# Kernel optimization log

Hardware: AMD Instinct MI355X
Metric: run time of the kernel (lower is better)

Reference implementation:

```python
import jax, jax.numpy as jnp
import numpy as np
from jax import lax

K = 100  # self.k in the module


def setup_inputs() -> dict:
    key = jax.random.key(0)
    k1, k2 = jax.random.split(key)
    query_batch = jax.random.normal(k1, (4, 64, 128), dtype=jnp.float32)  # [B,T,Z]
    targets = jax.random.normal(k2, (100000, 128), dtype=jnp.float32)     # [M,Z]
    return {"query_batch": query_batch, "targets": targets}


def _knn_emissions(query_batch, targets):
    # Brute-force L2 kNN (faiss.IndexFlatL2.search equivalent).
    # sqdist[b,t,m] = ||q_bt - target_m||^2
    qn = jnp.sum(query_batch * query_batch, -1)          # [B,T]
    tn = jnp.sum(targets * targets, -1)                  # [M]
    dots = jnp.einsum('btz,mz->btm', query_batch, targets)
    sqdist = qn[..., None] + tn[None, None, :] - 2.0 * dots  # [B,T,M]
    neg_d, idx = lax.top_k(-sqdist, K)                   # k smallest distances
    distances = -neg_d                                   # [B,T,K]
    # probabilities = exp(-d) / sum exp(-d)  == softmax(-d)
    emit_p = jax.nn.softmax(-distances, axis=-1)         # [B,T,K]
    states = targets[idx]                                # [B,T,K,Z]
    return emit_p, states


def _transition_probs(states):
    # Banded transitions: only between the K states of step t and step t+1.
    # transition_probability(a, b) = exp(-||a-b||^2)  (Gaussian L2 kernel)
    a = states[:, :-1]                                   # [B,T-1,K,Z]
    b = states[:, 1:]                                    # [B,T-1,K,Z]
    d = jnp.sum(a * a, -1)[..., :, None] + jnp.sum(b * b, -1)[..., None, :] \
        - 2.0 * jnp.einsum('btiz,btjz->btij', a, b)      # [B,T-1,K,K]
    return jnp.exp(-d)


def _viterbi_single(emit_p, trans_p):
    # emit_p [T,K], trans_p [T-1,K,K] -> best path indices [T] (int32)
    v0 = emit_p[0]

    def step(v, inp):
        tr, em = inp                                     # [K,K], [K]
        scores = v[:, None] * tr                         # [K,K]
        best = scores.max(axis=0)
        back = jnp.argmax(scores, axis=0)                # [K]
        v_new = best * em
        # rescale to avoid underflow over long T; argmax path unchanged
        v_new = v_new / jnp.maximum(v_new.max(), jnp.float32(1e-30))
        return v_new, back

    v_last, backptrs = lax.scan(step, v0, (trans_p, emit_p[1:]))
    last = jnp.argmax(v_last).astype(jnp.int32)

    def back_step(idx, bp):
        prev = bp[idx].astype(jnp.int32)
        return prev, prev

    _, path_head = lax.scan(back_step, last, backptrs, reverse=True)  # [T-1]
    return jnp.concatenate([path_head, last[None]])      # [T]


def reference(query_batch, targets):
    emit_p, states = _knn_emissions(query_batch, targets)
    trans_p = _transition_probs(states)
    paths = jax.vmap(_viterbi_single)(emit_p, trans_p)   # [B,T]
    # gather selected reference states: [B,T,Z]
    out = jnp.take_along_axis(states, paths[..., None, None], axis=2)[:, :, 0, :]
    return out
```

## Files before the change

kernel.cpp:

```cpp
#include <hip/hip_runtime.h>
#include <cfloat>
#include <climits>
#include <cstdint>
#include <cstddef>

#define ZD    128
#define NQ    256
#define NB    4
#define NT    64
#define KK    100
#define CAP   2048
#define NSAMP 4096
#define RANK  24
#define EPS   3.0f
#define SLABS 256
#define BKT   24
#define TROWS 64
#define QROWS 128
#define LPAD  136

typedef __attribute__((ext_vector_type(8))) short  short8;
typedef __attribute__((ext_vector_type(4))) float  floatx4;
typedef unsigned long long u64;

__device__ inline unsigned short f2bf(float f) {
  unsigned u = __builtin_bit_cast(unsigned, f);
  unsigned r = u + 0x7fffu + ((u >> 16) & 1u);
  return (unsigned short)(r >> 16);
}
__device__ inline unsigned fkey(float f) {
  unsigned u = __builtin_bit_cast(unsigned, f);
  unsigned m = (u & 0x80000000u) ? 0xFFFFFFFFu : 0x80000000u;
  return u ^ m;
}
__device__ inline float unfkey(unsigned k) {
  unsigned u = (k & 0x80000000u) ? (k ^ 0x80000000u) : ~k;
  return __builtin_bit_cast(float, u);
}

__global__ __launch_bounds__(256) void k0_norms(
    const float* __restrict__ Q, const float* __restrict__ T, int M,
    float* __restrict__ qn, float* __restrict__ tn) {
  int gid = blockIdx.x * 256 + threadIdx.x;
  if (gid < M) {
    const float* r = T + (size_t)gid * ZD;
    float s = 0.f;
    #pragma unroll
    for (int z4 = 0; z4 < 32; ++z4) {
      float4 v = *(const float4*)&r[z4 * 4];
      s = fmaf(v.x, v.x, s); s = fmaf(v.y, v.y, s);
      s = fmaf(v.z, v.z, s); s = fmaf(v.w, v.w, s);
    }
    tn[gid] = s;
  } else if (gid < M + NQ) {
    int q = gid - M;
    const float* r = Q + (size_t)q * ZD;
    float s = 0.f;
    #pragma unroll
    for (int z4 = 0; z4 < 32; ++z4) {
      float4 v = *(const float4*)&r[z4 * 4];
      s = fmaf(v.x, v.x, s); s = fmaf(v.y, v.y, s);
      s = fmaf(v.z, v.z, s); s = fmaf(v.w, v.w, s);
    }
    qn[q] = s;
  }
}

__global__ __launch_bounds__(256) void k1a_mfma(
    const float* __restrict__ Q, const float* __restrict__ T,
    const float* __restrict__ qn, const float* __restrict__ tn,
    float* __restrict__ sd_g) {
  __shared__ short Ts[TROWS * LPAD];
  __shared__ short Qs[QROWS * LPAD];
  const int tid = threadIdx.x;
  const int m0 = blockIdx.x * TROWS;
  const int qbase = blockIdx.y * QROWS;

  #pragma unroll
  for (int it = 0; it < 16; ++it) {
    int li = tid + it * 256;
    int row = li >> 5, z4 = li & 31;
    float4 v = *(const float4*)&Q[(size_t)(qbase + row) * ZD + z4 * 4];
    unsigned lo = (unsigned)f2bf(v.x) | ((unsigned)f2bf(v.y) << 16);
    unsigned hi = (unsigned)f2bf(v.z) | ((unsigned)f2bf(v.w) << 16);
    *(uint2*)&Qs[row * LPAD + z4 * 4] = make_uint2(lo, hi);
  }
  #pragma unroll
  for (int it = 0; it < 8; ++it) {
    int li = tid + it * 256;
    int row = li >> 5, z4 = li & 31;
    float4 v = *(const float4*)&T[(size_t)(m0 + row) * ZD + z4 * 4];
    unsigned lo = (unsigned)f2bf(v.x) | ((unsigned)f2bf(v.y) << 16);
    unsigned hi = (unsigned)f2bf(v.z) | ((unsigned)f2bf(v.w) << 16);
    *(uint2*)&Ts[row * LPAD + z4 * 4] = make_uint2(lo, hi);
  }
  __syncthreads();

  const int wave = tid >> 6;
  const int lane = tid & 63;
  const int quad = lane >> 4;
  const int n16  = lane & 15;

  floatx4 acc[8];
  #pragma unroll
  for (int qt = 0; qt < 8; ++qt) acc[qt] = (floatx4)0.f;
  #pragma unroll
  for (int ks = 0; ks < 4; ++ks) {
    short8 a = *(const short8*)&Ts[(wave * 16 + n16) * LPAD + ks * 32 + quad * 8];
    #pragma unroll
    for (int qt = 0; qt < 8; ++qt) {
      short8 b = *(const short8*)&Qs[(qt * 16 + n16) * LPAD + ks * 32 + quad * 8];
      acc[qt] = __builtin_amdgcn_mfma_f32_16x16x32_bf16(a, b, acc[qt], 0, 0, 0);
    }
  }

  const int mbase = m0 + wave * 16 + quad * 4;
  const float4 tnv = *(const float4*)&tn[mbase];
  #pragma unroll
  for (int qt = 0; qt < 8; ++qt) {
    const int q = qbase + qt * 16 + n16;
    const float base = qn[q];
    float4 dv;
    dv.x = fmaf(-2.0f, acc[qt][0], base + tnv.x);
    dv.y = fmaf(-2.0f, acc[qt][1], base + tnv.y);
    dv.z = fmaf(-2.0f, acc[qt][2], base + tnv.z);
    dv.w = fmaf(-2.0f, acc[qt][3], base + tnv.w);
    *(float4*)&sd_g[(size_t)q * NSAMP + mbase] = dv;
  }
}

__global__ __launch_bounds__(256) void k1b_pick(
    const float* __restrict__ sd_g, float* __restrict__ thr) {
  __shared__ float red[256];
  __shared__ int   hist[256];
  const int q = blockIdx.x, tid = threadIdx.x;
  const float* sd = sd_g + (size_t)q * NSAMP;
  float vals[16];
  float lm = FLT_MAX;
  #pragma unroll
  for (int k = 0; k < 16; ++k) {
    vals[k] = sd[k * 256 + tid];
    lm = fminf(lm, vals[k]);
  }
  red[tid] = lm;
  hist[tid] = 0;
  __syncthreads();
  for (int o = 128; o > 0; o >>= 1) {
    if (tid < o) red[tid] = fminf(red[tid], red[tid + o]);
    __syncthreads();
  }
  const float dmin = red[0];
  __syncthreads();
  #pragma unroll
  for (int k = 0; k < 16; ++k) {
    int b = (int)((vals[k] - dmin) * 3.2f);
    b = b < 0 ? 0 : (b > 255 ? 255 : b);
    atomicAdd(&hist[b], 1);
  }
  __syncthreads();
  if (tid == 0) {
    int cum = 0; float Tq = dmin + 80.0f;
    for (int b = 0; b < 256; ++b) {
      cum += hist[b];
      if (cum >= RANK) { Tq = dmin + (float)(b + 1) * 0.3125f; break; }
    }
    thr[q] = Tq;
  }
}

__global__ __launch_bounds__(256) void k2_mfma(
    const float* __restrict__ Q, const float* __restrict__ T, int M, int slabn,
    const float* __restrict__ qn, const float* __restrict__ tn,
    const float* __restrict__ thr,
    int* __restrict__ cnt2, int* __restrict__ sure2, int* __restrict__ cand) {
  __shared__ short Ts[TROWS * LPAD];
  __shared__ short Qs[QROWS * LPAD];
  __shared__ int   lcnt[QROWS];
  __shared__ int   lsure[QROWS];
  __shared__ int   lent[QROWS * BKT];
  const int tid = threadIdx.x;
  const int slab = blockIdx.x;
  const int qbase = blockIdx.y * QROWS;
  const int sbeg = slab * slabn;
  const int send = min(sbeg + slabn, M);

  #pragma unroll
  for (int it = 0; it < 16; ++it) {
    int li = tid + it * 256;
    int row = li >> 5, z4 = li & 31;
    float4 v = *(const float4*)&Q[(size_t)(qbase + row) * ZD + z4 * 4];
    unsigned lo = (unsigned)f2bf(v.x) | ((unsigned)f2bf(v.y) << 16);
    unsigned hi = (unsigned)f2bf(v.z) | ((unsigned)f2bf(v.w) << 16);
    *(uint2*)&Qs[row * LPAD + z4 * 4] = make_uint2(lo, hi);
  }
  if (tid < QROWS) { lcnt[tid] = 0; lsure[tid] = 0; }

  const int wave = tid >> 6;
  const int lane = tid & 63;
  const int quad = lane >> 4;
  const int n16  = lane & 15;

  for (int m0 = sbeg; m0 < send; m0 += TROWS) {
    __syncthreads();
    #pragma unroll
    for (int it = 0; it < 8; ++it) {
      int li = tid + it * 256;
      int row = li >> 5, z4 = li & 31;
      int m = m0 + row;
      float4 v = make_float4(0.f, 0.f, 0.f, 0.f);
      if (m < send) v = *(const float4*)&T[(size_t)m * ZD + z4 * 4];
      unsigned lo = (unsigned)f2bf(v.x) | ((unsigned)f2bf(v.y) << 16);
      unsigned hi = (unsigned)f2bf(v.z) | ((unsigned)f2bf(v.w) << 16);
      *(uint2*)&Ts[row * LPAD + z4 * 4] = make_uint2(lo, hi);
    }
    __syncthreads();

    floatx4 acc[8];
    #pragma unroll
    for (int qt = 0; qt < 8; ++qt) acc[qt] = (floatx4)0.f;
    #pragma unroll
    for (int ks = 0; ks < 4; ++ks) {
      short8 a = *(const short8*)&Ts[(wave * 16 + n16) * LPAD + ks * 32 + quad * 8];
      #pragma unroll
      for (int qt = 0; qt < 8; ++qt) {
        short8 b = *(const short8*)&Qs[(qt * 16 + n16) * LPAD + ks * 32 + quad * 8];
        acc[qt] = __builtin_amdgcn_mfma_f32_16x16x32_bf16(a, b, acc[qt], 0, 0, 0);
      }
    }

    const int mbase = m0 + wave * 16 + quad * 4;
    float4 tnv = make_float4(0.f, 0.f, 0.f, 0.f);
    if (mbase + 3 < M) tnv = *(const float4*)&tn[mbase];
    else {
      if (mbase + 0 < M) tnv.x = tn[mbase + 0];
      if (mbase + 1 < M) tnv.y = tn[mbase + 1];
      if (mbase + 2 < M) tnv.z = tn[mbase + 2];
    }
    const float tns[4] = {tnv.x, tnv.y, tnv.z, tnv.w};
    #pragma unroll
    for (int qt = 0; qt < 8; ++qt) {
      const int ql = qt * 16 + n16;
      const int q = qbase + ql;
      const float base = qn[q];
      const float Tq = thr[q];
      #pragma unroll
      for (int r = 0; r < 4; ++r) {
        const int m = mbase + r;
        float dap = fmaf(-2.0f, acc[qt][r], base + tns[r]);
        if (m < send && dap < Tq + EPS) {
          int pos = atomicAdd(&lcnt[ql], 1);
          if (pos < BKT) lent[ql * BKT + pos] = m;
          if (dap < Tq - EPS) atomicAdd(&lsure[ql], 1);
        }
      }
    }
  }
  __syncthreads();
  if (tid < QROWS) {
    cnt2 [(size_t)(qbase + tid) * SLABS + slab] = lcnt[tid];
    sure2[(size_t)(qbase + tid) * SLABS + slab] = lsure[tid];
  }
  for (int li = tid; li < QROWS * BKT; li += 256) {
    int ql = li / BKT, j = li % BKT;
    int c = lcnt[ql]; if (c > BKT) c = BKT;
    if (j < c)
      cand[((size_t)(qbase + ql) * SLABS + slab) * BKT + j] = lent[li];
  }
}

__global__ __launch_bounds__(256) void k3a_scan(
    const int* __restrict__ cnt2, const int* __restrict__ sure2,
    int* __restrict__ scanx, int* __restrict__ totals, int* __restrict__ validf) {
  const int q = blockIdx.x, tid = threadIdx.x;
  __shared__ int sscan[256];
  __shared__ int ssure, sovf;
  int c = cnt2[(size_t)q * SLABS + tid];
  int su = sure2[(size_t)q * SLABS + tid];
  if (tid == 0) { ssure = 0; sovf = 0; }
  __syncthreads();
  atomicAdd(&ssure, su);
  if (c > BKT) atomicOr(&sovf, 1);
  int val = c;
  sscan[tid] = val;
  __syncthreads();
  for (int o = 1; o < 256; o <<= 1) {
    int add = (tid >= o) ? sscan[tid - o] : 0;
    __syncthreads();
    val += add;
    sscan[tid] = val;
    __syncthreads();
  }
  scanx[(size_t)q * SLABS + tid] = val - c;
  const int total = sscan[255];
  if (tid == 0) {
    totals[q] = total;
    validf[q] = (sovf == 0 && ssure >= KK && total <= CAP) ? 1 : 0;
  }
}

__global__ __launch_bounds__(256) void k3b_rescore(
    const float* __restrict__ Q, const float* __restrict__ T,
    const float* __restrict__ qn, const float* __restrict__ tn,
    const int* __restrict__ cnt2, const int* __restrict__ cand,
    const int* __restrict__ scanx, const int* __restrict__ validf,
    u64* __restrict__ keys) {
  const int q = blockIdx.x, ch = blockIdx.y, tid = threadIdx.x;
  if (!validf[q]) return;
  __shared__ float qv[ZD];
  for (int z = tid; z < ZD; z += 256) qv[z] = Q[(size_t)q * ZD + z];
  __syncthreads();
  const float qnv = qn[q];
  const int slab = ch * 64 + (tid >> 2);
  const int lane = tid & 3;
  const int c = min(cnt2[(size_t)q * SLABS + slab], BKT);
  const int off = scanx[(size_t)q * SLABS + slab];
  for (int k = lane; k < c; k += 4) {
    int idx = cand[((size_t)q * SLABS + slab) * BKT + k];
    const float* r = T + (size_t)idx * ZD;
    float dot = 0.f;
    #pragma unroll 4
    for (int z4 = 0; z4 < 32; ++z4) {
      float4 v = *(const float4*)&r[z4 * 4];
      dot = fmaf(qv[z4 * 4 + 0], v.x, dot);
      dot = fmaf(qv[z4 * 4 + 1], v.y, dot);
      dot = fmaf(qv[z4 * 4 + 2], v.z, dot);
      dot = fmaf(qv[z4 * 4 + 3], v.w, dot);
    }
    float d = fmaf(-2.0f, dot, qnv + tn[idx]);
    keys[(size_t)q * CAP + off + k] = ((u64)fkey(d) << 32) | (unsigned)idx;
  }
}

__global__ __launch_bounds__(256) void k3c_select(
    const float* __restrict__ Q, const float* __restrict__ T, int M,
    const float* __restrict__ qn, const float* __restrict__ tn,
    const int* __restrict__ totals, const int* __restrict__ validf,
    const u64* __restrict__ keys_g,
    int* __restrict__ topi, float* __restrict__ emit) {
  __shared__ u64 key[CAP];
  __shared__ u64 buf[256];
  __shared__ unsigned redA[256], redB[256];
  __shared__ int hist[256];
  __shared__ int hscan[256];
  __shared__ float qv[ZD];
  __shared__ float cd[256];
  __shared__ float sdF[KK];
  __shared__ int   siF[KK];
  __shared__ float ebuf[KK];
  __shared__ float ssum;
  __shared__ int Bb, C2, ccnt, srcFlag;
  __shared__ unsigned kminS; __shared__ int shiftS;
  const int q = blockIdx.x, tid = threadIdx.x;
  const int total = totals[q];
  const bool valid = validf[q] != 0;

  if (valid) {
    for (int i = tid; i < CAP; i += 256)
      key[i] = (i < total) ? keys_g[(size_t)q * CAP + i] : ~0ULL;
    unsigned lmin = 0xFFFFFFFFu, lmax = 0u;
    for (int i = tid; i < total; i += 256) {
      unsigned h = (unsigned)(key[i] >> 32);
      lmin = min(lmin, h); lmax = max(lmax, h);
    }
    redA[tid] = lmin; redB[tid] = lmax;
    hist[tid] = 0;
    __syncthreads();
    for (int o = 128; o > 0; o >>= 1) {
      if (tid < o) {
        redA[tid] = min(redA[tid], redA[tid + o]);
        redB[tid] = max(redB[tid], redB[tid + o]);
      }
      __syncthreads();
    }
    if (tid == 0) {
      unsigned range = redB[0] - redA[0];
      int s = 0;
      while ((range >> s) > 255u) ++s;
      kminS = redA[0]; shiftS = s;
      ccnt = 0;
    }
    __syncthreads();
    const unsigned kmin = kminS; const int sh = shiftS;
    for (int i = tid; i < total; i += 256) {
      int b = (int)(((unsigned)(key[i] >> 32) - kmin) >> sh);
      atomicAdd(&hist[b], 1);
    }
    __syncthreads();
    int v0 = hist[tid];
    hscan[tid] = v0;
    __syncthreads();
    for (int o = 1; o < 256; o <<= 1) {
      int add = (tid >= o) ? hscan[tid - o] : 0;
      __syncthreads();
      v0 += add;
      hscan[tid] = v0;
      __syncthreads();
    }
    if (hscan[tid] >= KK && (tid == 0 || hscan[tid - 1] < KK)) {
      Bb = tid; C2 = hscan[tid];
    }
    __syncthreads();
    const int B = Bb, c2 = C2;
    if (c2 <= 256) {
      for (int i = tid; i < total; i += 256) {
        int b = (int)(((unsigned)(key[i] >> 32) - kmin) >> sh);
        if (b <= B) { int pos = atomicAdd(&ccnt, 1); buf[pos] = key[i]; }
      }
      __syncthreads();
      if (tid >= c2) buf[tid] = ~0ULL;
      __syncthreads();
      for (int k = 2; k <= 256; k <<= 1) {
        for (int j = k >> 1; j > 0; j >>= 1) {
          int x = tid ^ j;
          if (x > tid) {
            u64 a = buf[tid], b2 = buf[x];
            bool asc = ((tid & k) == 0);
            if ((a > b2) == asc) { buf[tid] = b2; buf[x] = a; }
          }
          __syncthreads();
        }
      }
      if (tid == 0) srcFlag = 0;
    } else {
      for (int k = 2; k <= CAP; k <<= 1) {
        for (int j = k >> 1; j > 0; j >>= 1) {
          for (int t = tid; t < CAP; t += 256) {
            int x = t ^ j;
            if (x > t) {
              u64 a = key[t], b2 = key[x];
              bool asc = ((t & k) == 0);
              if ((a > b2) == asc) { key[t] = b2; key[x] = a; }
            }
          }
          __syncthreads();
        }
      }
      if (tid == 0) srcFlag = 1;
    }
    __syncthreads();
  } else {
    for (int z = tid; z < ZD; z += 256) qv[z] = Q[(size_t)q * ZD + z];
    if (tid == 0) {
      for (int k = 0; k < KK; ++k) { sdF[k] = FLT_MAX; siF[k] = INT_MAX; }
      srcFlag = 0;
    }
    __syncthreads();
    const float qnv = qn[q];
    for (int base = 0; base < M; base += 256) {
      int m = base + tid; float d = FLT_MAX;
      if (m < M) {
        const float* r = T + (size_t)m * ZD;
        float dot = 0.f;
        for (int z = 0; z < ZD; ++z) dot = fmaf(qv[z], r[z], dot);
        d = fmaf(-2.0f, dot, qnv + tn[m]);
      }
      cd[tid] = d;
      __syncthreads();
      if (tid == 0) {
        for (int e = 0; e < 256; ++e) {
          float dd = cd[e]; int mm = base + e;
          if (dd < sdF[KK - 1] || (dd == sdF[KK - 1] && mm < siF[KK - 1])) {
            int pos = KK - 1;
            while (pos > 0 && (sdF[pos - 1] > dd || (sdF[pos - 1] == dd && siF[pos - 1] > mm))) {
              sdF[pos] = sdF[pos - 1]; siF[pos] = siF[pos - 1]; --pos;
            }
            sdF[pos] = dd; siF[pos] = mm;
          }
        }
      }
      __syncthreads();
    }
    if (tid < KK) buf[tid] = ((u64)fkey(sdF[tid]) << 32) | (unsigned)siF[tid];
    __syncthreads();
  }

  const int sf = srcFlag;
  if (tid == 0) {
    u64 k0v = sf ? key[0] : buf[0];
    float d0 = unfkey((unsigned)(k0v >> 32));
    float sum = 0.f;
    for (int k = 0; k < KK; ++k) {
      u64 kk = sf ? key[k] : buf[k];
      float e = expf(d0 - unfkey((unsigned)(kk >> 32)));
      ebuf[k] = e; sum += e;
    }
    ssum = sum;
  }
  __syncthreads();
  if (tid < KK) {
    u64 kk = sf ? key[tid] : buf[tid];
    emit[(size_t)q * KK + tid] = ebuf[tid] / ssum;
    topi[(size_t)q * KK + tid] = (int)(kk & 0xFFFFFFFFu);
  }
}

__global__ __launch_bounds__(256) void k4_trans(
    const float* __restrict__ T, const int* __restrict__ topi,
    float* __restrict__ trans) {
  const int bt = blockIdx.x;
  const int b = bt / (NT - 1), t = bt % (NT - 1);
  const int* iA = topi + (size_t)(b * NT + t) * KK;
  const int* iB = topi + (size_t)(b * NT + t + 1) * KK;
  __shared__ float As[KK * 132];
  __shared__ float Bs[20 * 132];
  __shared__ float an[KK];
  __shared__ float bn[20];
  const int tid = threadIdx.x;
  for (int li = tid; li < KK * 32; li += 256) {
    int row = li >> 5, z4 = li & 31;
    float4 v = *(const float4*)&T[(size_t)iA[row] * ZD + z4 * 4];
    *(float4*)&As[row * 132 + z4 * 4] = v;
  }
  __syncthreads();
  if (tid < KK) {
    float s = 0.f;
    for (int z = 0; z < ZD; ++z) s = fmaf(As[tid * 132 + z], As[tid * 132 + z], s);
    an[tid] = s;
  }
  for (int c = 0; c < 5; ++c) {
    __syncthreads();
    for (int li = tid; li < 20 * 32; li += 256) {
      int row = li >> 5, z4 = li & 31;
      float4 v = *(const float4*)&T[(size_t)iB[c * 20 + row] * ZD + z4 * 4];
      *(float4*)&Bs[row * 132 + z4 * 4] = v;
    }
    __syncthreads();
    if (tid < 20) {
      float s = 0.f;
      for (int z = 0; z < ZD; ++z) s = fmaf(Bs[tid * 132 + z], Bs[tid * 132 + z], s);
      bn[tid] = s;
    }
    __syncthreads();
    if (tid < 125) {
      const int i0 = (tid / 5) * 4, j0 = (tid % 5) * 4;
      float acc[16];
      #pragma unroll
      for (int x = 0; x < 16; ++x) acc[x] = 0.f;
      for (int z4 = 0; z4 < 32; ++z4) {
        float4 a[4], bb[4];
        #pragma unroll
        for (int r = 0; r < 4; ++r) a[r] = *(const float4*)&As[(i0 + r) * 132 + z4 * 4];
        #pragma unroll
        for (int s = 0; s < 4; ++s) bb[s] = *(const float4*)&Bs[(j0 + s) * 132 + z4 * 4];
        #pragma unroll
        for (int r = 0; r < 4; ++r) {
          #pragma unroll
          for (int s = 0; s < 4; ++s) {
            acc[r * 4 + s] = fmaf(a[r].x, bb[s].x, acc[r * 4 + s]);
            acc[r * 4 + s] = fmaf(a[r].y, bb[s].y, acc[r * 4 + s]);
            acc[r * 4 + s] = fmaf(a[r].z, bb[s].z, acc[r * 4 + s]);
            acc[r * 4 + s] = fmaf(a[r].w, bb[s].w, acc[r * 4 + s]);
          }
        }
      }
      float* trow = trans + (size_t)bt * KK * KK;
      #pragma unroll
      for (int r = 0; r < 4; ++r)
        for (int s = 0; s < 4; ++s) {
          float d = fmaf(-2.0f, acc[r * 4 + s], an[i0 + r] + bn[j0 + s]);
          trow[(i0 + r) * KK + c * 20 + j0 + s] = expf(-d);
        }
    }
  }
}

__global__ __launch_bounds__(256) void k5_viterbi(
    const float* __restrict__ T, const int* __restrict__ topi,
    const float* __restrict__ emit, const float* __restrict__ trans,
    float* __restrict__ out) {
  const int b = blockIdx.x, tid = threadIdx.x;
  __shared__ float trS[KK * KK];
  __shared__ float v[KK], vn[KK];
  __shared__ float pb[200];
  __shared__ int   pi[200];
  __shared__ int   bpS[(NT - 1) * KK];
  __shared__ int   path[NT];
  __shared__ float maxsh;
  __shared__ int   zflag;

  float4 r[10];
  {
    const float* tr0 = trans + (size_t)(b * (NT - 1)) * KK * KK;
    #pragma unroll
    for (int i = 0; i < 10; ++i) {
      int li = tid + i * 256;
      if (li < 2500) r[i] = *(const float4*)&tr0[li * 4];
    }
  }
  if (tid < KK) v[tid] = emit[(size_t)(b * NT) * KK + tid];
  if (tid == 0) zflag = 0;
  __syncthreads();

  for (int t = 1; t < NT; ++t) {
    const int zf = zflag;
    if (zf == 0) {
      #pragma unroll
      for (int i = 0; i < 10; ++i) {
        int li = tid + i * 256;
        if (li < 2500) *(float4*)&trS[li * 4] = r[i];
      }
      __syncthreads();
      if (t < NT - 1) {
        const float* trn = trans + (size_t)(b * (NT - 1) + t) * KK * KK;
        #pragma unroll
        for (int i = 0; i < 10; ++i) {
          int li = tid + i * 256;
          if (li < 2500) r[i] = *(const float4*)&trn[li * 4];
        }
      }
      if (tid < 200) {
        const int j = tid % 100, half = tid / 100;
        const int ia = half * 50, ibnd = ia + 50;
        float best = -FLT_MAX; int bi = ia;
        for (int i = ia; i < ibnd; ++i) {
          float s = v[i] * trS[i * KK + j];
          if (s > best) { best = s; bi = i; }
        }
        pb[tid] = best; pi[tid] = bi;
      }
      __syncthreads();
      if (tid < KK) {
        float b0 = pb[tid], b1 = pb[100 + tid];
        int   i0 = pi[tid], i1 = pi[100 + tid];
        float best = b0; int bi = i0;
        if (b1 > b0) { best = b1; bi = i1; }
        vn[tid] = best * emit[(size_t)(b * NT + t) * KK + tid];
        bpS[(t - 1) * KK + tid] = bi;
      }
      __syncthreads();
      if (tid == 0) {
        float m = vn[0];
        for (int j = 1; j < KK; ++j) m = fmaxf(m, vn[j]);
        maxsh = m;
        if (m == 0.0f) zflag = 1;
      }
      __syncthreads();
      if (tid < KK) v[tid] = vn[tid] / fmaxf(maxsh, 1e-30f);
    } else {
      if (tid < KK) bpS[(t - 1) * KK + tid] = 0;
    }
    __syncthreads();
  }
  if (tid == 0) {
    float best = -FLT_MAX; int last = 0;
    for (int j = 0; j < KK; ++j) if (v[j] > best) { best = v[j]; last = j; }
    path[NT - 1] = last;
    for (int tt = NT - 2; tt >= 0; --tt)
      path[tt] = bpS[tt * KK + path[tt + 1]];
  }
  __syncthreads();
  for (int li = tid; li < NT * ZD; li += 256) {
    int t = li >> 7, z = li & 127;
    out[(size_t)(b * NT + t) * ZD + z] =
        T[(size_t)topi[(size_t)(b * NT + t) * KK + path[t]] * ZD + z];
  }
}

extern "C" void kernel_launch(void* const* d_in, const int* in_sizes, int n_in,
                              void* d_out, int out_size, void* d_ws, size_t ws_size,
                              hipStream_t stream) {
  const float* Q = (const float*)d_in[0];
  const float* T = (const float*)d_in[1];
  float* out = (float*)d_out;
  const int M = in_sizes[1] / ZD;
  const int slabn = (M + SLABS - 1) / SLABS;

  char* p = (char*)d_ws;
  auto alloc = [&](size_t bytes) -> char* {
    char* r = p; p += (bytes + 511) & ~(size_t)511; return r;
  };
  float* qn     = (float*)alloc((size_t)NQ * 4);
  float* tn     = (float*)alloc((size_t)M * 4);
  float* thr    = (float*)alloc((size_t)NQ * 4);
  float* sd_g   = (float*)alloc((size_t)NQ * NSAMP * 4);
  int*   cnt2   = (int*)  alloc((size_t)NQ * SLABS * 4);
  int*   sure2  = (int*)  alloc((size_t)NQ * SLABS * 4);
  int*   cand   = (int*)  alloc((size_t)NQ * SLABS * BKT * 4);
  int*   scanx  = (int*)  alloc((size_t)NQ * SLABS * 4);
  int*   totals = (int*)  alloc((size_t)NQ * 4);
  int*   validf = (int*)  alloc((size_t)NQ * 4);
  u64*   keys   = (u64*)  alloc((size_t)NQ * CAP * 8);
  int*   topi   = (int*)  alloc((size_t)NQ * KK * 4);
  float* emit   = (float*)alloc((size_t)NQ * KK * 4);
  float* trans  = (float*)alloc((size_t)NB * (NT - 1) * KK * KK * 4);

  const int g0 = (M + NQ + 255) / 256;
  k0_norms<<<g0, 256, 0, stream>>>(Q, T, M, qn, tn);
  dim3 g1a(NSAMP / TROWS, NQ / QROWS);
  k1a_mfma<<<g1a, 256, 0, stream>>>(Q, T, qn, tn, sd_g);
  k1b_pick<<<NQ, 256, 0, stream>>>(sd_g, thr);
  dim3 g2(SLABS, NQ / QROWS);
  k2_mfma<<<g2, 256, 0, stream>>>(Q, T, M, slabn, qn, tn, thr, cnt2, sure2, cand);
  k3a_scan<<<NQ, 256, 0, stream>>>(cnt2, sure2, scanx, totals, validf);
  dim3 g3b(NQ, 4);
  k3b_rescore<<<g3b, 256, 0, stream>>>(Q, T, qn, tn, cnt2, cand, scanx, validf, keys);
  k3c_select<<<NQ, 256, 0, stream>>>(Q, T, M, qn, tn, totals, validf, keys, topi, emit);
  k4_trans<<<NB * (NT - 1), 256, 0, stream>>>(T, topi, trans);
  k5_viterbi<<<NB, 256, 0, stream>>>(T, topi, emit, trans, out);
}
```

Measured before the change: 284.1 us.

## Prefetch target tiles into registers in k2 and retile k4 transition GEMM

In the brute-force distance kernel, the next 64-row target tile is loaded into registers while the MFMA work on the current tile runs, hiding global load latency. An occupancy hint of 4 blocks is added to its launch bounds. The transition kernel now loads all 100 B states at once and uses all 256 threads with a 7x7 strided tile per thread, replacing the 5-chunk loop where only 125 threads worked. The k2 prefetch adds register pressure, which may conflict with the occupancy hint. The larger k4 shared footprint (about 106KB) limits how many blocks fit per CU.

After: 255.3 us. 10.2% less time.

```diff
diff --git a/kernel.cpp b/kernel.cpp
--- a/kernel.cpp
+++ b/kernel.cpp
@@ -168,7 +168,7 @@
   }
 }
 
-__global__ __launch_bounds__(256) void k2_mfma(
+__global__ __launch_bounds__(256, 4) void k2_mfma(
     const float* __restrict__ Q, const float* __restrict__ T, int M, int slabn,
     const float* __restrict__ qn, const float* __restrict__ tn,
     const float* __restrict__ thr,
@@ -200,20 +200,37 @@
   const int quad = lane >> 4;
   const int n16  = lane & 15;
 
+  float4 pf[8];
+  #pragma unroll
+  for (int it = 0; it < 8; ++it) {
+    int li = tid + it * 256;
+    int row = li >> 5, z4 = li & 31;
+    int m = sbeg + row;
+    pf[it] = make_float4(0.f, 0.f, 0.f, 0.f);
+    if (m < send) pf[it] = *(const float4*)&T[(size_t)m * ZD + z4 * 4];
+  }
+
   for (int m0 = sbeg; m0 < send; m0 += TROWS) {
     __syncthreads();
     #pragma unroll
     for (int it = 0; it < 8; ++it) {
       int li = tid + it * 256;
       int row = li >> 5, z4 = li & 31;
-      int m = m0 + row;
-      float4 v = make_float4(0.f, 0.f, 0.f, 0.f);
-      if (m < send) v = *(const float4*)&T[(size_t)m * ZD + z4 * 4];
-      unsigned lo = (unsigned)f2bf(v.x) | ((unsigned)f2bf(v.y) << 16);
-      unsigned hi = (unsigned)f2bf(v.z) | ((unsigned)f2bf(v.w) << 16);
+      unsigned lo = (unsigned)f2bf(pf[it].x) | ((unsigned)f2bf(pf[it].y) << 16);
+      unsigned hi = (unsigned)f2bf(pf[it].z) | ((unsigned)f2bf(pf[it].w) << 16);
       *(uint2*)&Ts[row * LPAD + z4 * 4] = make_uint2(lo, hi);
     }
     __syncthreads();
+    if (m0 + TROWS < send) {
+      #pragma unroll
+      for (int it = 0; it < 8; ++it) {
+        int li = tid + it * 256;
+        int row = li >> 5, z4 = li & 31;
+        int m = m0 + TROWS + row;
+        pf[it] = make_float4(0.f, 0.f, 0.f, 0.f);
+        if (m < send) pf[it] = *(const float4*)&T[(size_t)m * ZD + z4 * 4];
+      }
+    }
 
     floatx4 acc[8];
     #pragma unroll
@@ -502,64 +519,65 @@
   const int* iA = topi + (size_t)(b * NT + t) * KK;
   const int* iB = topi + (size_t)(b * NT + t + 1) * KK;
   __shared__ float As[KK * 132];
-  __shared__ float Bs[20 * 132];
+  __shared__ float Bs[KK * 132];
   __shared__ float an[KK];
-  __shared__ float bn[20];
+  __shared__ float bn[KK];
   const int tid = threadIdx.x;
   for (int li = tid; li < KK * 32; li += 256) {
     int row = li >> 5, z4 = li & 31;
-    float4 v = *(const float4*)&T[(size_t)iA[row] * ZD + z4 * 4];
-    *(float4*)&As[row * 132 + z4 * 4] = v;
+    *(float4*)&As[row * 132 + z4 * 4] = *(const float4*)&T[(size_t)iA[row] * ZD + z4 * 4];
+    *(float4*)&Bs[row * 132 + z4 * 4] = *(const float4*)&T[(size_t)iB[row] * ZD + z4 * 4];
   }
   __syncthreads();
   if (tid < KK) {
     float s = 0.f;
     for (int z = 0; z < ZD; ++z) s = fmaf(As[tid * 132 + z], As[tid * 132 + z], s);
     an[tid] = s;
-  }
-  for (int c = 0; c < 5; ++c) {
-    __syncthreads();
-    for (int li = tid; li < 20 * 32; li += 256) {
-      int row = li >> 5, z4 = li & 31;
-      float4 v = *(const float4*)&T[(size_t)iB[c * 20 + row] * ZD + z4 * 4];
-      *(float4*)&Bs[row * 132 + z4 * 4] = v;
-    }
-    __syncthreads();
-    if (tid < 20) {
-      float s = 0.f;
-      for (int z = 0; z < ZD; ++z) s = fmaf(Bs[tid * 132 + z], Bs[tid * 132 + z], s);
-      bn[tid] = s;
-    }
-    __syncthreads();
-    if (tid < 125) {
-      const int i0 = (tid / 5) * 4, j0 = (tid % 5) * 4;
-      float acc[16];
+  } else if (tid < 2 * KK) {
+    int r = tid - KK;
+    float s = 0.f;
+    for (int z = 0; z < ZD; ++z) s = fmaf(Bs[r * 132 + z], Bs[r * 132 + z], s);
+    bn[r] = s;
+  }
+  __syncthreads();
+  const int tx = tid & 15, ty = tid >> 4;
+  float acc[7][7];
+  #pragma unroll
+  for (int k = 0; k < 7; ++k)
+    #pragma unroll
+    for (int m = 0; m < 7; ++m) acc[k][m] = 0.f;
+  int rr[7], cc[7];
+  #pragma unroll
+  for (int k = 0; k < 7; ++k) { rr[k] = min(ty + 16 * k, KK - 1); cc[k] = min(tx + 16 * k, KK - 1); }
+  for (int z4 = 0; z4 < 32; ++z4) {
+    float4 a[7], bb[7];
+    #pragma unroll
+    for (int k = 0; k < 7; ++k) a[k] = *(const float4*)&As[rr[k] * 132 + z4 * 4];
+    #pragma unroll
+    for (int m = 0; m < 7; ++m) bb[m] = *(const float4*)&Bs[cc[m] * 132 + z4 * 4];
+    #pragma unroll
+    for (int k = 0; k < 7; ++k)
       #pragma unroll
-      for (int x = 0; x < 16; ++x) acc[x] = 0.f;
-      for (int z4 = 0; z4 < 32; ++z4) {
-        float4 a[4], bb[4];
-        #pragma unroll
-        for (int r = 0; r < 4; ++r) a[r] = *(const float4*)&As[(i0 + r) * 132 + z4 * 4];
-        #pragma unroll
-        for (int s = 0; s < 4; ++s) bb[s] = *(const float4*)&Bs[(j0 + s) * 132 + z4 * 4];
-        #pragma unroll
-        for (int r = 0; r < 4; ++r) {
-          #pragma unroll
-          for (int s = 0; s < 4; ++s) {
-            acc[r * 4 + s] = fmaf(a[r].x, bb[s].x, acc[r * 4 + s]);
-            acc[r * 4 + s] = fmaf(a[r].y, bb[s].y, acc[r * 4 + s]);
-            acc[r * 4 + s] = fmaf(a[r].z, bb[s].z, acc[r * 4 + s]);
-            acc[r * 4 + s] = fmaf(a[r].w, bb[s].w, acc[r * 4 + s]);
-          }
+      for (int m = 0; m < 7; ++m) {
+        acc[k][m] = fmaf(a[k].x, bb[m].x, acc[k][m]);
+        acc[k][m] = fmaf(a[k].y, bb[m].y, acc[k][m]);
+        acc[k][m] = fmaf(a[k].z, bb[m].z, acc[k][m]);
+        acc[k][m] = fmaf(a[k].w, bb[m].w, acc[k][m]);
+      }
+  }
+  float* trow = trans + (size_t)bt * KK * KK;
+  #pragma unroll
+  for (int k = 0; k < 7; ++k) {
+    int r = ty + 16 * k;
+    if (r < KK) {
+      #pragma unroll
+      for (int m = 0; m < 7; ++m) {
+        int c = tx + 16 * m;
+        if (c < KK) {
+          float d = fmaf(-2.0f, acc[k][m], an[r] + bn[c]);
+          trow[r * KK + c] = expf(-d);
         }
       }
-      float* trow = trans + (size_t)bt * KK * KK;
-      #pragma unroll
-      for (int r = 0; r < 4; ++r)
-        for (int s = 0; s < 4; ++s) {
-          float d = fmaf(-2.0f, acc[r * 4 + s], an[i0 + r] + bn[j0 + s]);
-          trow[(i0 + r) * KK + c * 20 + j0 + s] = expf(-d);
-        }
     }
   }
 }
```
